# Optimization experiments

Hardware: AMD Instinct MI355X
Metric: run time of the kernel (lower is better)

## Reference

```python
import jax, jax.numpy as jnp
import numpy as np


def setup_inputs() -> dict:
    key = jax.random.key(0)
    ks = jax.random.split(key, 12)
    B, T, S, D, A, E, L, V = 32, 64, 64, 1024, 512, 256, 1024, 12000
    s = 0.02  # weight scale for numerical stability
    return {
        "targets": jax.random.randint(ks[0], (B, T), 0, V),
        "options": jax.random.normal(ks[1], (B, S, D), jnp.float32),
        "h0": jax.random.normal(ks[2], (B, L), jnp.float32),
        "c0": jnp.zeros((B, L), jnp.float32),
        "emb": jax.random.normal(ks[3], (V, E), jnp.float32) * s,
        "W1": jax.random.normal(ks[4], (L, A), jnp.float32) * s,
        "b1": jnp.zeros((A,), jnp.float32),
        "W2": jax.random.normal(ks[5], (D, A), jnp.float32) * s,
        "b2": jnp.zeros((A,), jnp.float32),
        "Va": jax.random.normal(ks[6], (A, 1), jnp.float32) * s,
        "bVa": jnp.zeros((1,), jnp.float32),
        "Wx": jax.random.normal(ks[7], (D + E, 4 * L), jnp.float32) * s,
        "Wh": jax.random.normal(ks[8], (L, 4 * L), jnp.float32) * s,
        "bl": jnp.zeros((4 * L,), jnp.float32),
        "Wd": jax.random.normal(ks[9], (L, V), jnp.float32) * s,
        "bd": jnp.zeros((V,), jnp.float32),
    }


def reference(targets, options, h0, c0, emb, W1, b1, W2, b2, Va, bVa,
              Wx, Wh, bl, Wd, bd):
    L = h0.shape[-1]
    # W2(options) is step-invariant: hoist out of recurrent loop. [B,S,A]
    opt_proj = jnp.einsum('bsd,da->bsa', options, W2) + b2

    def step(carry, x_ids):
        h, c = carry
        # Bahdanau attention: score = V(tanh(W1(h) + W2(options)))
        score = jnp.tanh(h @ W1 + b1)[:, None, :] + opt_proj        # [B,S,A]
        score = jnp.einsum('bsa,ao->bso', score, Va) + bVa          # [B,S,1]
        w = jax.nn.softmax(score, axis=1)                           # [B,S,1]
        context = jnp.sum(w * options, axis=1)                      # [B,D]
        x = jnp.concatenate([context, emb[x_ids]], axis=-1)         # [B,D+E]
        # Keras LSTM cell, gate order i, f, g, o
        z = x @ Wx + h @ Wh + bl                                    # [B,4L]
        i, f, g, o = jnp.split(z, 4, axis=-1)
        c = jax.nn.sigmoid(f) * c + jax.nn.sigmoid(i) * jnp.tanh(g)
        h = jax.nn.sigmoid(o) * jnp.tanh(c)
        probs = jax.nn.softmax(h @ Wd + bd, axis=-1)                # [B,V]
        return (h, c), (probs, w[..., 0])

    (h, c), (out, attn) = jax.lax.scan(step, (h0, c0), targets.T)
    output = jnp.transpose(out, (1, 0, 2))   # [B,T,V]
    attention = attn[-1][..., None]          # last-step attention weights [B,S,1]
    return output, h, c, attention
```

## Files before the change

### kernel.cpp

```cpp
#include <hip/hip_runtime.h>
#include <math.h>


typedef __bf16 bf16;
typedef _Float16 fp16;
typedef __attribute__((ext_vector_type(8))) _Float16 fp16x8;
typedef __attribute__((ext_vector_type(4))) _Float16 fp16x4;
typedef __attribute__((ext_vector_type(4))) float f32x4;

constexpr int B = 32, T = 64, S = 64, D = 1024, A = 512, E = 256, L = 1024, V = 12000;
constexpr int G = 4096;
constexpr size_t N_PROBS = (size_t)B * T * V;

__device__ inline void load_lds16(const void* g, void* l) {
  __builtin_amdgcn_global_load_lds(
      (const __attribute__((address_space(1))) unsigned int*)g,
      (__attribute__((address_space(3))) unsigned int*)l, 16, 0, 0);
}


__global__ void k_v2(const float* __restrict__ W2, const float* __restrict__ Va,
                     float* __restrict__ v2) {
  int gw = (blockIdx.x * blockDim.x + threadIdx.x) >> 6;
  int lane = threadIdx.x & 63;
  if (gw >= D) return;
  float acc = 0.f;
  for (int a = lane; a < A; a += 64) acc += W2[(size_t)gw * A + a] * Va[a];
  #pragma unroll
  for (int off = 32; off; off >>= 1) acc += __shfl_down(acc, off);
  if (lane == 0) v2[gw] = acc;
}

__global__ void k_score(const float* __restrict__ options, const float* __restrict__ v2,
                        float* __restrict__ w) {
  int row = (blockIdx.x * blockDim.x + threadIdx.x) >> 6;
  int lane = threadIdx.x & 63;
  if (row >= B * S) return;
  const float* orow = options + (size_t)row * D;
  float acc = 0.f;
  for (int d = lane; d < D; d += 64) acc += orow[d] * v2[d];
  #pragma unroll
  for (int off = 32; off; off >>= 1) acc += __shfl_down(acc, off);
  if (lane == 0) w[row] = acc;
}

__global__ __launch_bounds__(256) void k_attnctx(
    const float* __restrict__ options, const float* __restrict__ wat,
    float* __restrict__ oattn, float* __restrict__ ctx) {
  __shared__ float sw[64];
  const int b = blockIdx.x, tid = threadIdx.x;
  if (tid < 64) {
    float v = wat[b * 64 + tid];
    float m = v;
    #pragma unroll
    for (int off = 32; off; off >>= 1) m = fmaxf(m, __shfl_xor(m, off));
    float e = expf(v - m);
    float s = e;
    #pragma unroll
    for (int off = 32; off; off >>= 1) s += __shfl_xor(s, off);
    float res = e / s;
    sw[tid] = res;
    oattn[b * 64 + tid] = res;
  }
  __syncthreads();
  for (int d = tid; d < D; d += 256) {
    float acc = 0.f;
    #pragma unroll 8
    for (int s = 0; s < 64; ++s)
      acc += sw[s] * options[((size_t)(b * 64 + s)) * D + d];
    ctx[b * D + d] = acc;
  }
}

__global__ __launch_bounds__(256) void k_cx_part(
    const float* __restrict__ ctx, const float* __restrict__ Wx,
    float* __restrict__ cxp) {
  const int jt = blockIdx.x & 15;
  const int bg = (blockIdx.x >> 4) & 3;
  const int kc = blockIdx.x >> 6;
  const int j = jt * 256 + threadIdx.x;
  const int b0 = bg * 8, d0 = kc * 128;
  float acc[8];
  #pragma unroll
  for (int bb = 0; bb < 8; ++bb) acc[bb] = 0.f;
  for (int d = 0; d < 128; ++d) {
    float wv = Wx[(size_t)(d0 + d) * G + j];
    #pragma unroll
    for (int bb = 0; bb < 8; ++bb)
      acc[bb] = fmaf(ctx[(b0 + bb) * D + d0 + d], wv, acc[bb]);
  }
  #pragma unroll
  for (int bb = 0; bb < 8; ++bb)
    cxp[((size_t)kc * 32 + b0 + bb) * G + j] = acc[bb];
}

__global__ void k_cx_reduce(const float* __restrict__ cxp, const float* __restrict__ bl,
                            float* __restrict__ cx) {
  int i = blockIdx.x * 256 + threadIdx.x;
  float s = bl[i & 4095];
  #pragma unroll
  for (int kc = 0; kc < 8; ++kc) s += cxp[(size_t)kc * 131072 + i];
  cx[i] = s;
}


__global__ void k_eg(const int* __restrict__ targets, const float* __restrict__ emb,
                     fp16* __restrict__ eg) {
  int r = blockIdx.x, e = threadIdx.x;
  int tok = targets[r];
  eg[(size_t)r * E + e] = (fp16)emb[(size_t)tok * E + e];
}

__global__ __launch_bounds__(256) void k_wx2t(const float* __restrict__ Wx,
                                              fp16* __restrict__ t16) {
  __shared__ float s[64][65];
  const int et = blockIdx.x >> 6, jt = blockIdx.x & 63;
  const int e0 = et * 64, j0 = jt * 64;
  const int tid = threadIdx.x;
  const int jj = tid & 63;
  #pragma unroll
  for (int k = 0; k < 16; ++k) {
    int ee = k * 4 + (tid >> 6);
    s[ee][jj] = Wx[(size_t)(D + e0 + ee) * G + j0 + jj];
  }
  __syncthreads();
  const int jc = tid >> 2, eq = tid & 3;
  fp16x8 o0, o1;
  #pragma unroll
  for (int i = 0; i < 8; ++i) {
    o0[i] = (fp16)s[eq * 16 + i][jc];
    o1[i] = (fp16)s[eq * 16 + 8 + i][jc];
  }
  size_t dst = (size_t)(j0 + jc) * E + e0 + eq * 16;
  *(fp16x8*)(t16 + dst) = o0;
  *(fp16x8*)(t16 + dst + 8) = o1;
}

__global__ __launch_bounds__(256) void k_whp(const float* __restrict__ Wh,
                                             fp16* __restrict__ p) {
  __shared__ float s[64][65];
  const int lt = blockIdx.x & 15, ct = blockIdx.x >> 4;
  const int l0 = lt * 64, c0 = ct * 64;
  const int tid = threadIdx.x;
  const int cc = tid & 63;
  #pragma unroll
  for (int k = 0; k < 16; ++k) {
    int ll = k * 4 + (tid >> 6);
    s[ll][cc] = Wh[(size_t)(l0 + ll) * G + c0 + cc];
  }
  __syncthreads();
  const int c = tid >> 2, lq = tid & 3;
  const int col = c0 + c, g = col >> 10, jj = col & 1023;
  const int rowp = ((jj >> 2) << 4) + (g << 2) + (jj & 3);
  fp16x8 o0, o1;
  #pragma unroll
  for (int i = 0; i < 8; ++i) {
    o0[i] = (fp16)s[lq * 16 + i][c];
    o1[i] = (fp16)s[lq * 16 + 8 + i][c];
  }
  size_t dst = (size_t)rowp * L + l0 + lq * 16;
  *(fp16x8*)(p + dst) = o0;
  *(fp16x8*)(p + dst + 8) = o1;
}

__global__ void k_h0split(const float* __restrict__ h0, const float* __restrict__ c0,
                          fp16* __restrict__ h16, float* __restrict__ cst,
                          float* __restrict__ hf32) {
  int i = blockIdx.x * 256 + threadIdx.x;
  float x = h0[i];
  h16[i] = (fp16)x;
  hf32[i] = x;
  cst[i] = c0[i];
}

__global__ __launch_bounds__(256) void k_pre_mfma(
    const fp16* __restrict__ Ag, const fp16* __restrict__ Bg,
    const float* __restrict__ cx, fp16* __restrict__ prep) {
  __shared__ __align__(16) char lds[32768];
  char* sA = lds;
  char* sB = lds + 16384;
  const int bid = blockIdx.x;
  const int swz = (bid & 7) * 64 + (bid >> 3);
  const int mt = swz >> 5, nt = swz & 31;
  const int m0 = mt * 128, n0 = nt * 128;
  const int tid = threadIdx.x, w = tid >> 6, lane = tid & 63;
  const int wr = w >> 1, wc = w & 1;

  f32x4 acc[4][4];
  #pragma unroll
  for (int i = 0; i < 4; ++i)
    #pragma unroll
    for (int j = 0; j < 4; ++j) acc[i][j] = (f32x4){0.f, 0.f, 0.f, 0.f};

  int rowc[4], sloc[4];
  #pragma unroll
  for (int i = 0; i < 4; ++i) {
    int c = i * 4 + w;
    rowc[i] = c * 8 + (lane >> 3);
    sloc[i] = (lane & 7) ^ (rowc[i] & 7);
  }

  for (int kk = 0; kk < 4; ++kk) {
    if (kk) __syncthreads();
    const char* ga = (const char*)Ag + kk * 128;
    const char* gb = (const char*)Bg + kk * 128;
    #pragma unroll
    for (int i = 0; i < 4; ++i) {
      int c = i * 4 + w;
      load_lds16(ga + (size_t)(m0 + rowc[i]) * 512 + sloc[i] * 16, sA + c * 1024);
      load_lds16(gb + (size_t)(n0 + rowc[i]) * 512 + sloc[i] * 16, sB + c * 1024);
    }
    __syncthreads();
    #pragma unroll
    for (int ks = 0; ks < 2; ++ks) {
      fp16x8 av[4], bv[4];
      #pragma unroll
      for (int f = 0; f < 4; ++f) {
        int ra = wr * 64 + f * 16 + (lane & 15);
        int ca = (ks * 4 + (lane >> 4)) ^ (ra & 7);
        av[f] = *(const fp16x8*)(sA + ra * 128 + ca * 16);
        int rb = wc * 64 + f * 16 + (lane & 15);
        int cb = (ks * 4 + (lane >> 4)) ^ (rb & 7);
        bv[f] = *(const fp16x8*)(sB + rb * 128 + cb * 16);
      }
      #pragma unroll
      for (int fm = 0; fm < 4; ++fm)
        #pragma unroll
        for (int fn = 0; fn < 4; ++fn)
          acc[fm][fn] = __builtin_amdgcn_mfma_f32_16x16x32_f16(
              av[fm], bv[fn], acc[fm][fn], 0, 0, 0);
    }
  }

  const int r0o = m0 + wr * 64 + ((lane >> 4) << 2);
  const int c0o = n0 + wc * 64 + (lane & 15);
  #pragma unroll
  for (int fn = 0; fn < 4; ++fn) {
    int colg = c0o + fn * 16;
    int g = colg >> 10, jj = colg & 1023;
    int jb = jj >> 2, jo = jj & 3;
    #pragma unroll
    for (int fm = 0; fm < 4; ++fm) {
      #pragma unroll
      for (int r = 0; r < 4; ++r) {
        int row = r0o + fm * 16 + r;
        int b = row >> 6, t = row & 63;
        float v = acc[fm][fn][r] + cx[(size_t)b * G + colg];
        prep[(((size_t)t * 256 + jb) * 32 + b) * 16 + jo * 4 + g] = (fp16)v;
      }
    }
  }
}

__global__ __launch_bounds__(256) void k_step6(
    const fp16* __restrict__ Whp, const fp16* __restrict__ prep,
    const fp16* __restrict__ Aprev, int Ars,
    float* __restrict__ cst, float* __restrict__ hf32,
    fp16* __restrict__ Hb16, int t) {
  __shared__ f32x4 zred[4][64];
  const int jb = blockIdx.x >> 1, bh = blockIdx.x & 1;
  const int tid = threadIdx.x;
  const int w = tid >> 6, lane = tid & 63;
  const int fr = lane & 15, kc = lane >> 4;

  f32x4 a0 = (f32x4){0.f, 0.f, 0.f, 0.f}, a1 = a0;
  const fp16* bb = Whp + (size_t)(jb * 16 + fr) * 1024 + w * 256 + kc * 8;
  const fp16* aa = Aprev + (size_t)(bh * 16 + fr) * Ars + w * 256 + kc * 8;
  #pragma unroll
  for (int kk = 0; kk < 8; kk += 2) {
    a0 = __builtin_amdgcn_mfma_f32_16x16x32_f16(
        *(const fp16x8*)(aa + kk * 32), *(const fp16x8*)(bb + kk * 32), a0, 0, 0, 0);
    a1 = __builtin_amdgcn_mfma_f32_16x16x32_f16(
        *(const fp16x8*)(aa + (kk + 1) * 32), *(const fp16x8*)(bb + (kk + 1) * 32), a1, 0, 0, 0);
  }
  f32x4 zv;
  #pragma unroll
  for (int q = 0; q < 4; ++q) zv[q] = a0[q] + a1[q];
  zred[w][lane] = zv;
  __syncthreads();

  const int b_local = tid >> 4, col = tid & 15;
  const int b = bh * 16 + b_local;
  const int g = col >> 2, jo = col & 3;
  const int lane2 = ((b_local >> 2) << 4) | col;
  const int reg = b_local & 3;
  float z = zred[0][lane2][reg] + zred[1][lane2][reg]
          + zred[2][lane2][reg] + zred[3][lane2][reg];
  z += (float)prep[(((size_t)t * 256 + jb) * 32 + b) * 16 + jo * 4 + g];
  float act;
  if (g == 2) act = 1.f - 2.f / (1.f + __expf(2.f * z));
  else        act = 1.f / (1.f + __expf(-z));
  float x4 = __shfl_xor(act, 4);
  float za = (g & 1) ? x4 : act;
  float zb = (g & 1) ? act : x4;
  float za2 = __shfl_xor(za, 8);
  float zb2 = __shfl_xor(zb, 8);
  const bool lo = (g < 2);
  float Ai = lo ? za : za2;
  float Af = lo ? zb : zb2;
  float Ag_ = lo ? za2 : za;
  float Ao = lo ? zb2 : zb;
  if (g == 0) {
    const int gj = jb * 4 + jo;
    float cp = cst[b * 1024 + gj];
    float cn = Af * cp + Ai * Ag_;
    float th = 1.f - 2.f / (1.f + __expf(2.f * cn));
    float hn = Ao * th;
    cst[b * 1024 + gj] = cn;
    Hb16[((size_t)b * 64 + t) * 1024 + gj] = (fp16)hn;
    if (t == T - 1) hf32[b * 1024 + gj] = hn;
  }
}

__global__ __launch_bounds__(256) void k_wdt(const float* __restrict__ Wd,
                                             fp16* __restrict__ Wdt) {
  __shared__ float s[64][65];
  const int lt = blockIdx.x & 15;
  const int vt = blockIdx.x >> 4;
  const int l0 = lt * 64, v0 = vt * 64;
  const int tid = threadIdx.x;
  const int lv = tid & 63;
  #pragma unroll
  for (int k = 0; k < 16; ++k) {
    int ll = k * 4 + (tid >> 6);
    int v = v0 + lv;
    s[ll][lv] = (v < V) ? Wd[(size_t)(l0 + ll) * V + v] : 0.f;
  }
  __syncthreads();
  const int vv = tid >> 2, lq = tid & 3;
  fp16x8 o0, o1;
  #pragma unroll
  for (int j = 0; j < 8; ++j) {
    o0[j] = (fp16)s[lq * 16 + j][vv];
    o1[j] = (fp16)s[lq * 16 + 8 + j][vv];
  }
  fp16* dst = Wdt + (size_t)(v0 + vv) * 1024 + l0 + lq * 16;
  *(fp16x8*)dst = o0;
  *(fp16x8*)(dst + 8) = o1;
}

__global__ __launch_bounds__(256) void k_logits_mfma(
    const fp16* __restrict__ Ag, const fp16* __restrict__ Btg,
    const float* __restrict__ bd, float* __restrict__ out) {
  __shared__ __align__(16) char lds[65536];
  char* sA = lds;
  char* sB = lds + 16384;
  const int bid = blockIdx.x;
  const int wg = (bid & 7) * 188 + (bid >> 3);
  const int nt = wg >> 4, mt = wg & 15;
  const int m0 = mt * 128, n0 = nt * 128;
  const int tid = threadIdx.x, w = tid >> 6, lane = tid & 63;
  const int wr = w >> 1, wc = w & 1;

  f32x4 acc[4][4];
  #pragma unroll
  for (int i = 0; i < 4; ++i)
    #pragma unroll
    for (int j = 0; j < 4; ++j) acc[i][j] = (f32x4){0.f, 0.f, 0.f, 0.f};

  int rowc[4], sloc[4];
  #pragma unroll
  for (int i = 0; i < 4; ++i) {
    int c = i * 4 + w;
    rowc[i] = c * 8 + (lane >> 3);
    sloc[i] = (lane & 7) ^ (rowc[i] & 7);
  }

  for (int kk = 0; kk < 16; ++kk) {
    if (kk) __syncthreads();
    const char* ga = (const char*)Ag + kk * 128;
    const char* gb = (const char*)Btg + kk * 128;
    #pragma unroll
    for (int i = 0; i < 4; ++i) {
      int c = i * 4 + w;
      load_lds16(ga + (size_t)(m0 + rowc[i]) * 2048 + sloc[i] * 16, sA + c * 1024);
      load_lds16(gb + (size_t)(n0 + rowc[i]) * 2048 + sloc[i] * 16, sB + c * 1024);
    }
    __syncthreads();
    #pragma unroll
    for (int ks = 0; ks < 2; ++ks) {
      fp16x8 av[4], bv[4];
      #pragma unroll
      for (int f = 0; f < 4; ++f) {
        int ra = wr * 64 + f * 16 + (lane & 15);
        int ca = (ks * 4 + (lane >> 4)) ^ (ra & 7);
        av[f] = *(const fp16x8*)(sA + ra * 128 + ca * 16);
        int rb = wc * 64 + f * 16 + (lane & 15);
        int cb = (ks * 4 + (lane >> 4)) ^ (rb & 7);
        bv[f] = *(const fp16x8*)(sB + rb * 128 + cb * 16);
      }
      #pragma unroll
      for (int fm = 0; fm < 4; ++fm)
        #pragma unroll
        for (int fn = 0; fn < 4; ++fn)
          acc[fm][fn] = __builtin_amdgcn_mfma_f32_16x16x32_f16(
              av[fm], bv[fn], acc[fm][fn], 0, 0, 0);
    }
  }

  __syncthreads();
  float* ctile = (float*)lds;
  const int c0o = n0 + wc * 64 + (lane & 15);
  #pragma unroll
  for (int fn = 0; fn < 4; ++fn) {
    int colg = c0o + fn * 16;
    float bv = (colg < V) ? bd[colg] : 0.f;
    int col = wc * 64 + fn * 16 + (lane & 15);
    #pragma unroll
    for (int fm = 0; fm < 4; ++fm) {
      int row = wr * 64 + fm * 16 + ((lane >> 4) << 2);
      #pragma unroll
      for (int r = 0; r < 4; ++r)
        ctile[(row + r) * 128 + col] = acc[fm][fn][r] + bv;
    }
  }
  __syncthreads();
  #pragma unroll
  for (int it = 0; it < 16; ++it) {
    int idx = it * 256 + tid;
    int row = idx >> 5, ch = idx & 31;
    int colg = n0 + ch * 4;
    if (colg < V)
      *(float4*)&out[(size_t)(m0 + row) * V + colg] = *(float4*)&ctile[row * 128 + ch * 4];
  }
}

__global__ __launch_bounds__(256) void k_softmax(float* __restrict__ logits) {
  __shared__ float srow[V];
  __shared__ float sred[4];
  float* row = logits + (size_t)blockIdx.x * V;
  const int tid = threadIdx.x;
  const float4* rv = (const float4*)row;
  float4* sv = (float4*)srow;
  float m = -3.4e38f;
  for (int i = tid; i < 3000; i += 256) {
    float4 x = rv[i];
    sv[i] = x;
    m = fmaxf(fmaxf(m, fmaxf(x.x, x.y)), fmaxf(x.z, x.w));
  }
  #pragma unroll
  for (int off = 32; off; off >>= 1) m = fmaxf(m, __shfl_xor(m, off));
  if ((tid & 63) == 0) sred[tid >> 6] = m;
  __syncthreads();
  const float M = fmaxf(fmaxf(sred[0], sred[1]), fmaxf(sred[2], sred[3]));
  float s = 0.f;
  for (int i = tid; i < 3000; i += 256) {
    float4 x = sv[i];
    x.x = __expf(x.x - M); x.y = __expf(x.y - M);
    x.z = __expf(x.z - M); x.w = __expf(x.w - M);
    sv[i] = x;
    s += x.x + x.y + x.z + x.w;
  }
  #pragma unroll
  for (int off = 32; off; off >>= 1) s += __shfl_xor(s, off);
  __syncthreads();
  if ((tid & 63) == 0) sred[tid >> 6] = s;
  __syncthreads();
  const float inv = 1.f / (sred[0] + sred[1] + sred[2] + sred[3]);
  float4* ov = (float4*)row;
  for (int i = tid; i < 3000; i += 256) {
    float4 x = sv[i];
    x.x *= inv; x.y *= inv; x.z *= inv; x.w *= inv;
    ov[i] = x;
  }
}

__global__ void k_finalize(const float* __restrict__ hf32, const float* __restrict__ cst,
                           float* __restrict__ oh, float* __restrict__ oc) {
  int i = blockIdx.x * 256 + threadIdx.x;
  if (i < B * L) {
    oh[i] = hf32[i];
    oc[i] = cst[i];
  }
}


extern "C" void kernel_launch(void* const* d_in, const int* in_sizes, int n_in,
                              void* d_out, int out_size, void* d_ws, size_t ws_size,
                              hipStream_t stream) {
  const int*   targets = (const int*)d_in[0];
  const float* options = (const float*)d_in[1];
  const float* h0      = (const float*)d_in[2];
  const float* c0      = (const float*)d_in[3];
  const float* emb     = (const float*)d_in[4];
  const float* W2      = (const float*)d_in[7];
  const float* Va      = (const float*)d_in[9];
  const float* Wx      = (const float*)d_in[11];
  const float* Wh      = (const float*)d_in[12];
  const float* bl      = (const float*)d_in[13];
  const float* Wd      = (const float*)d_in[14];
  const float* bd      = (const float*)d_in[15];

  float* out      = (float*)d_out;
  float* out_h    = out + N_PROBS;
  float* out_c    = out_h + (size_t)B * L;
  float* out_attn = out_c + (size_t)B * L;

  char* wsb = (char*)d_ws;
  float* v2     = (float*)(wsb);
  float* wat    = (float*)(wsb + 4096);
  float* ctx    = (float*)(wsb + 12288);
  float* cx     = (float*)(wsb + 143360);
  float* cst    = (float*)(wsb + 667648);
  fp16*  hA     = (fp16*)(wsb + 798720);
  float* hf32   = (float*)(wsb + 929792);
  fp16*  Eg16   = (fp16*)(wsb + 1191936);
  fp16*  Wx2t16 = (fp16*)(wsb + 2240512);
  fp16*  Hb16   = (fp16*)(wsb + 1191936);
  fp16*  Whp    = (fp16*)(wsb + 7483392);
  fp16*  prep   = (fp16*)(wsb + 15872000);
  float* cxp    = (float*)(wsb + 15872000);
  fp16*  Wdt    = (fp16*)(wsb + 7483392);

  k_v2<<<256, 256, 0, stream>>>(W2, Va, v2);
  k_score<<<512, 256, 0, stream>>>(options, v2, wat);
  k_attnctx<<<32, 256, 0, stream>>>(options, wat, out_attn, ctx);
  k_cx_part<<<512, 256, 0, stream>>>(ctx, Wx, cxp);
  k_cx_reduce<<<512, 256, 0, stream>>>(cxp, bl, cx);

  k_eg<<<2048, 256, 0, stream>>>(targets, emb, Eg16);
  k_wx2t<<<256, 256, 0, stream>>>(Wx, Wx2t16);
  k_whp<<<1024, 256, 0, stream>>>(Wh, Whp);

  k_pre_mfma<<<512, 256, 0, stream>>>(Eg16, Wx2t16, cx, prep);
  k_h0split<<<128, 256, 0, stream>>>(h0, c0, hA, cst, hf32);

  for (int t = 0; t < T; ++t) {
    const fp16* Aprev = (t == 0) ? hA : (Hb16 + (size_t)(t - 1) * 1024);
    int Ars = (t == 0) ? 1024 : 65536;
    k_step6<<<512, 256, 0, stream>>>(Whp, prep, Aprev, Ars, cst, hf32, Hb16, t);
  }

  k_wdt<<<188 * 16, 256, 0, stream>>>(Wd, Wdt);
  k_logits_mfma<<<1504, 256, 0, stream>>>(Hb16, Wdt, bd, out);
  k_softmax<<<B * T, 256, 0, stream>>>(out);
  k_finalize<<<128, 256, 0, stream>>>(hf32, cst, out_h, out_c);
}
```

Baseline: 607.5 us.

## Restructure LSTM step kernel, ping-pong hidden state, shrink logits epilogue LDS

The recurrent step kernel now has each 512-thread block cover all 32 batch rows for one gate-column block, so every Wh fragment is loaded once and reused across both batch halves. A compact ping-pong fp16 hidden buffer replaces the strided reads from the history array. The step kernel writes final h and c straight into the outputs, which removes the finalize kernel and the fp32 hidden copy. The logits kernel halves its LDS by writing the output tile in two passes, which may raise occupancy at the cost of an extra barrier.

```diff
diff --git a/kernel.cpp b/kernel.cpp
--- a/kernel.cpp
+++ b/kernel.cpp
@@ -2,10 +2,8 @@
 #include <math.h>
 
 
-typedef __bf16 bf16;
 typedef _Float16 fp16;
 typedef __attribute__((ext_vector_type(8))) _Float16 fp16x8;
-typedef __attribute__((ext_vector_type(4))) _Float16 fp16x4;
 typedef __attribute__((ext_vector_type(4))) float f32x4;
 
 constexpr int B = 32, T = 64, S = 64, D = 1024, A = 512, E = 256, L = 1024, V = 12000;
@@ -164,12 +162,9 @@
 }
 
 __global__ void k_h0split(const float* __restrict__ h0, const float* __restrict__ c0,
-                          fp16* __restrict__ h16, float* __restrict__ cst,
-                          float* __restrict__ hf32) {
+                          fp16* __restrict__ h16, float* __restrict__ cst) {
   int i = blockIdx.x * 256 + threadIdx.x;
-  float x = h0[i];
-  h16[i] = (fp16)x;
-  hf32[i] = x;
+  h16[i] = (fp16)h0[i];
   cst[i] = c0[i];
 }
 
@@ -252,40 +247,40 @@
   }
 }
 
-__global__ __launch_bounds__(256) void k_step6(
+__global__ __launch_bounds__(512) void k_step7(
     const fp16* __restrict__ Whp, const fp16* __restrict__ prep,
-    const fp16* __restrict__ Aprev, int Ars,
-    float* __restrict__ cst, float* __restrict__ hf32,
-    fp16* __restrict__ Hb16, int t) {
-  __shared__ f32x4 zred[4][64];
-  const int jb = blockIdx.x >> 1, bh = blockIdx.x & 1;
+    const fp16* __restrict__ hin, fp16* __restrict__ hout,
+    float* __restrict__ cst, fp16* __restrict__ Hb16,
+    float* __restrict__ out_h, float* __restrict__ out_c, int t) {
+  __shared__ f32x4 zred[16][64];
+  const int jb = blockIdx.x;
   const int tid = threadIdx.x;
   const int w = tid >> 6, lane = tid & 63;
   const int fr = lane & 15, kc = lane >> 4;
 
-  f32x4 a0 = (f32x4){0.f, 0.f, 0.f, 0.f}, a1 = a0;
-  const fp16* bb = Whp + (size_t)(jb * 16 + fr) * 1024 + w * 256 + kc * 8;
-  const fp16* aa = Aprev + (size_t)(bh * 16 + fr) * Ars + w * 256 + kc * 8;
-  #pragma unroll
-  for (int kk = 0; kk < 8; kk += 2) {
+  f32x4 a0 = (f32x4){0.f, 0.f, 0.f, 0.f};
+  f32x4 a1 = a0;
+  const fp16* bb = Whp + (size_t)(jb * 16 + fr) * 1024;
+  #pragma unroll
+  for (int kk = 0; kk < 4; ++kk) {
+    const int k0 = (w * 4 + kk) * 32 + kc * 8;
+    fp16x8 bv = *(const fp16x8*)(bb + k0);
     a0 = __builtin_amdgcn_mfma_f32_16x16x32_f16(
-        *(const fp16x8*)(aa + kk * 32), *(const fp16x8*)(bb + kk * 32), a0, 0, 0, 0);
+        *(const fp16x8*)(hin + (size_t)fr * 1024 + k0), bv, a0, 0, 0, 0);
     a1 = __builtin_amdgcn_mfma_f32_16x16x32_f16(
-        *(const fp16x8*)(aa + (kk + 1) * 32), *(const fp16x8*)(bb + (kk + 1) * 32), a1, 0, 0, 0);
-  }
-  f32x4 zv;
-  #pragma unroll
-  for (int q = 0; q < 4; ++q) zv[q] = a0[q] + a1[q];
-  zred[w][lane] = zv;
-  __syncthreads();
-
-  const int b_local = tid >> 4, col = tid & 15;
-  const int b = bh * 16 + b_local;
+        *(const fp16x8*)(hin + (size_t)(16 + fr) * 1024 + k0), bv, a1, 0, 0, 0);
+  }
+  zred[w * 2 + 0][lane] = a0;
+  zred[w * 2 + 1][lane] = a1;
+  __syncthreads();
+
+  const int b = tid >> 4, col = tid & 15;
   const int g = col >> 2, jo = col & 3;
-  const int lane2 = ((b_local >> 2) << 4) | col;
-  const int reg = b_local & 3;
-  float z = zred[0][lane2][reg] + zred[1][lane2][reg]
-          + zred[2][lane2][reg] + zred[3][lane2][reg];
+  const int lane2 = (((b & 15) >> 2) << 4) | col;
+  const int reg = b & 3, m = b >> 4;
+  float z = 0.f;
+  #pragma unroll
+  for (int ww = 0; ww < 8; ++ww) z += zred[ww * 2 + m][lane2][reg];
   z += (float)prep[(((size_t)t * 256 + jb) * 32 + b) * 16 + jo * 4 + g];
   float act;
   if (g == 2) act = 1.f - 2.f / (1.f + __expf(2.f * z));
@@ -302,13 +297,18 @@
   float Ao = lo ? zb2 : zb;
   if (g == 0) {
     const int gj = jb * 4 + jo;
-    float cp = cst[b * 1024 + gj];
+    const int ci = b * 1024 + gj;
+    float cp = cst[ci];
     float cn = Af * cp + Ai * Ag_;
     float th = 1.f - 2.f / (1.f + __expf(2.f * cn));
     float hn = Ao * th;
-    cst[b * 1024 + gj] = cn;
+    cst[ci] = cn;
+    hout[ci] = (fp16)hn;
     Hb16[((size_t)b * 64 + t) * 1024 + gj] = (fp16)hn;
-    if (t == T - 1) hf32[b * 1024 + gj] = hn;
+    if (t == T - 1) {
+      out_h[ci] = hn;
+      out_c[ci] = cn;
+    }
   }
 }
 
@@ -342,7 +342,7 @@
 __global__ __launch_bounds__(256) void k_logits_mfma(
     const fp16* __restrict__ Ag, const fp16* __restrict__ Btg,
     const float* __restrict__ bd, float* __restrict__ out) {
-  __shared__ __align__(16) char lds[65536];
+  __shared__ __align__(16) char lds[32768];
   char* sA = lds;
   char* sB = lds + 16384;
   const int bid = blockIdx.x;
@@ -398,30 +398,39 @@
     }
   }
 
-  __syncthreads();
   float* ctile = (float*)lds;
-  const int c0o = n0 + wc * 64 + (lane & 15);
+  float bvv[4];
   #pragma unroll
   for (int fn = 0; fn < 4; ++fn) {
-    int colg = c0o + fn * 16;
-    float bv = (colg < V) ? bd[colg] : 0.f;
-    int col = wc * 64 + fn * 16 + (lane & 15);
-    #pragma unroll
-    for (int fm = 0; fm < 4; ++fm) {
-      int row = wr * 64 + fm * 16 + ((lane >> 4) << 2);
+    int colg = n0 + wc * 64 + fn * 16 + (lane & 15);
+    bvv[fn] = (colg < V) ? bd[colg] : 0.f;
+  }
+  #pragma unroll
+  for (int p = 0; p < 2; ++p) {
+    __syncthreads();
+    if (wr == p) {
+      const int col = wc * 64 + (lane & 15);
       #pragma unroll
-      for (int r = 0; r < 4; ++r)
-        ctile[(row + r) * 128 + col] = acc[fm][fn][r] + bv;
-    }
-  }
-  __syncthreads();
-  #pragma unroll
-  for (int it = 0; it < 16; ++it) {
-    int idx = it * 256 + tid;
-    int row = idx >> 5, ch = idx & 31;
-    int colg = n0 + ch * 4;
-    if (colg < V)
-      *(float4*)&out[(size_t)(m0 + row) * V + colg] = *(float4*)&ctile[row * 128 + ch * 4];
+      for (int fn = 0; fn < 4; ++fn) {
+        #pragma unroll
+        for (int fm = 0; fm < 4; ++fm) {
+          int row = fm * 16 + ((lane >> 4) << 2);
+          #pragma unroll
+          for (int r = 0; r < 4; ++r)
+            ctile[(row + r) * 128 + col + fn * 16] = acc[fm][fn][r] + bvv[fn];
+        }
+      }
+    }
+    __syncthreads();
+    #pragma unroll
+    for (int it = 0; it < 8; ++it) {
+      int idx = it * 256 + tid;
+      int row = idx >> 5, ch = idx & 31;
+      int colg = n0 + ch * 4;
+      if (colg < V)
+        *(float4*)&out[(size_t)(m0 + p * 64 + row) * V + colg] =
+            *(float4*)&ctile[row * 128 + ch * 4];
+    }
   }
 }
 
@@ -462,15 +471,6 @@
     float4 x = sv[i];
     x.x *= inv; x.y *= inv; x.z *= inv; x.w *= inv;
     ov[i] = x;
-  }
-}
-
-__global__ void k_finalize(const float* __restrict__ hf32, const float* __restrict__ cst,
-                           float* __restrict__ oh, float* __restrict__ oc) {
-  int i = blockIdx.x * 256 + threadIdx.x;
-  if (i < B * L) {
-    oh[i] = hf32[i];
-    oc[i] = cst[i];
   }
 }
 
@@ -503,7 +503,7 @@
   float* cx     = (float*)(wsb + 143360);
   float* cst    = (float*)(wsb + 667648);
   fp16*  hA     = (fp16*)(wsb + 798720);
-  float* hf32   = (float*)(wsb + 929792);
+  fp16*  hB     = (fp16*)(wsb + 864256);
   fp16*  Eg16   = (fp16*)(wsb + 1191936);
   fp16*  Wx2t16 = (fp16*)(wsb + 2240512);
   fp16*  Hb16   = (fp16*)(wsb + 1191936);
@@ -523,16 +523,16 @@
   k_whp<<<1024, 256, 0, stream>>>(Wh, Whp);
 
   k_pre_mfma<<<512, 256, 0, stream>>>(Eg16, Wx2t16, cx, prep);
-  k_h0split<<<128, 256, 0, stream>>>(h0, c0, hA, cst, hf32);
+  k_h0split<<<128, 256, 0, stream>>>(h0, c0, hA, cst);
 
   for (int t = 0; t < T; ++t) {
-    const fp16* Aprev = (t == 0) ? hA : (Hb16 + (size_t)(t - 1) * 1024);
-    int Ars = (t == 0) ? 1024 : 65536;
-    k_step6<<<512, 256, 0, stream>>>(Whp, prep, Aprev, Ars, cst, hf32, Hb16, t);
+    const fp16* hin = (t & 1) ? hB : hA;
+    fp16* hout = (t & 1) ? hA : hB;
+    k_step7<<<256, 512, 0, stream>>>(Whp, prep, hin, hout, cst, Hb16,
+                                     out_h, out_c, t);
   }
 
   k_wdt<<<188 * 16, 256, 0, stream>>>(Wd, Wdt);
   k_logits_mfma<<<1504, 256, 0, stream>>>(Hb16, Wdt, bd, out);
   k_softmax<<<B * T, 256, 0, stream>>>(out);
-  k_finalize<<<128, 256, 0, stream>>>(hf32, cst, out_h, out_c);
-}
+}
```

Result: faster. 571.1 us (-6.0%).
